# Kernel tuning notes

Measured on AMD Instinct MI355X. Metric: run time of the kernel, lower is better.

The kernel has to match this reference:

```python
import jax, jax.numpy as jnp
import numpy as np

EXCHANGE_RATIO = 0.5


def setup_inputs() -> dict:
    key = jax.random.key(0)
    k1, k2, k3, k4 = jax.random.split(key, 4)
    B, C, L = 8, 512, 4096
    x1 = jax.random.normal(k1, (B, C, L), dtype=jnp.float32)
    x2 = jax.random.normal(k2, (B, C, L), dtype=jnp.float32)
    bn1 = jax.random.normal(k3, (C,), dtype=jnp.float32)
    bn2 = jax.random.normal(k4, (C,), dtype=jnp.float32)
    return {"x1": x1, "x2": x2, "bn1": bn1, "bn2": bn2}


def _nontop_indices(bn, topk):
    # channels NOT in topk of |bn|, in ascending index order (matches torch
    # boolean-mask indexing semantics)
    a = jnp.abs(bn)
    C = bn.shape[0]
    _, idx = jax.lax.top_k(a, topk)
    mask = jnp.zeros((C,), dtype=bool).at[idx].set(True)
    # stable argsort of bool puts False (non-top) first, in ascending index order
    nontop = jnp.argsort(mask, stable=True)[: C - topk]
    return nontop


def reference(x1, x2, bn1, bn2):
    C = bn1.shape[0]
    topk = int(C * (1.0 - EXCHANGE_RATIO))  # static: 256
    nontop1 = _nontop_indices(bn1, topk)
    nontop2 = _nontop_indices(bn2, topk)
    # y1 keeps x1's top channels, takes x2's non-top channels (order-aligned)
    y1 = x1.at[:, nontop1, :].set(x2[:, nontop2, :])
    # y2 keeps x2's top channels, takes x1's non-top channels
    y2 = x2.at[:, nontop2, :].set(x1[:, nontop1, :])
    return (y1, y2)
```

## Files before the change

kernel.cpp:

```cpp
#include <hip/hip_runtime.h>
#include <math.h>

#define C_CH   512
#define TOPK   256
#define B_N    8
#define L_LEN  4096
#define L4     (L_LEN / 4)
#define NVEC   (B_N * C_CH * L4)

__global__ void build_maps(const float* __restrict__ bn1,
                           const float* __restrict__ bn2,
                           int* __restrict__ map1,
                           int* __restrict__ map2) {
    __shared__ float a1[C_CH], a2[C_CH];
    __shared__ int istop1[C_CH], istop2[C_CH];
    __shared__ int nontop1[C_CH], nontop2[C_CH];
    const int t = threadIdx.x;
    a1[t] = fabsf(bn1[t]);
    a2[t] = fabsf(bn2[t]);
    __syncthreads();

    const float v1 = a1[t], v2 = a2[t];
    int r1 = 0, r2 = 0;
    for (int j = 0; j < C_CH; ++j) {
        const float b1 = a1[j], b2 = a2[j];
        r1 += (b1 > v1) || (b1 == v1 && j < t);
        r2 += (b2 > v2) || (b2 == v2 && j < t);
    }
    const int top1 = (r1 < TOPK);
    const int top2 = (r2 < TOPK);
    istop1[t] = top1;
    istop2[t] = top2;
    __syncthreads();

    int p1 = -1, p2 = -1;
    if (!top1) {
        int p = 0;
        for (int j = 0; j < t; ++j) p += !istop1[j];
        p1 = p;
        nontop1[p] = t;
    }
    if (!top2) {
        int p = 0;
        for (int j = 0; j < t; ++j) p += !istop2[j];
        p2 = p;
        nontop2[p] = t;
    }
    __syncthreads();

    map1[t] = top1 ? t : (C_CH + nontop2[p1]);
    map2[t] = top2 ? t : (C_CH + nontop1[p2]);
}

__global__ __launch_bounds__(256) void exchange_copy(
        const float4* __restrict__ x1,
        const float4* __restrict__ x2,
        const int* __restrict__ map1,
        const int* __restrict__ map2,
        float4* __restrict__ y1,
        float4* __restrict__ y2) {
    const int idx = blockIdx.x * blockDim.x + threadIdx.x;
    const int off = idx & (L4 - 1);
    const int row = idx >> 10;
    const int c   = row & (C_CH - 1);
    const int b   = row >> 9;

    const int m1 = map1[c];
    const int m2 = map2[c];

    const float4* s1 = (m1 < C_CH) ? x1 : x2;
    const float4* s2 = (m2 < C_CH) ? x2 : x1;
    const int c1 = m1 & (C_CH - 1);
    const int c2 = m2 & (C_CH - 1);

    const int base_b = b << 9;
    y1[idx] = s1[(((base_b | c1) << 10) | off)];
    y2[idx] = s2[(((base_b | c2) << 10) | off)];
}

extern "C" void kernel_launch(void* const* d_in, const int* in_sizes, int n_in,
                              void* d_out, int out_size, void* d_ws, size_t ws_size,
                              hipStream_t stream) {
    const float* x1  = (const float*)d_in[0];
    const float* x2  = (const float*)d_in[1];
    const float* bn1 = (const float*)d_in[2];
    const float* bn2 = (const float*)d_in[3];

    float* y1 = (float*)d_out;
    float* y2 = (float*)d_out + (B_N * C_CH * L_LEN);

    int* map1 = (int*)d_ws;
    int* map2 = map1 + C_CH;

    build_maps<<<1, C_CH, 0, stream>>>(bn1, bn2, map1, map2);

    const int threads = 256;
    const int blocks = NVEC / threads;
    exchange_copy<<<blocks, threads, 0, stream>>>(
        (const float4*)x1, (const float4*)x2, map1, map2,
        (float4*)y1, (float4*)y2);
}
```

Before: 275.8 us.

## Use ballot prefix sums in map build and row-per-block batched copy

The map-building kernel now finds the position of each non-top channel with wavefront ballot, popcount and a small per-wave prefix sum, replacing the O(C) serial scan in each thread, and packs the two abs arrays into one float2 shared array. The copy kernel gives each block one full row, so the map lookup happens once per row, and each thread issues four float4 loads per source before storing them, raising memory-level parallelism. The grid shrinks to 4096 blocks, each doing more work per thread, which may reduce latency hiding if occupancy limits the number of loads in flight.

```diff
diff --git a/kernel.cpp b/kernel.cpp
--- a/kernel.cpp
+++ b/kernel.cpp
@@ -6,50 +6,54 @@
 #define B_N    8
 #define L_LEN  4096
 #define L4     (L_LEN / 4)
-#define NVEC   (B_N * C_CH * L4)
+#define ROWS   (B_N * C_CH)
 
-__global__ void build_maps(const float* __restrict__ bn1,
-                           const float* __restrict__ bn2,
-                           int* __restrict__ map1,
-                           int* __restrict__ map2) {
-    __shared__ float a1[C_CH], a2[C_CH];
-    __shared__ int istop1[C_CH], istop2[C_CH];
-    __shared__ int nontop1[C_CH], nontop2[C_CH];
+__global__ __launch_bounds__(C_CH) void build_maps(
+        const float* __restrict__ bn1,
+        const float* __restrict__ bn2,
+        int* __restrict__ map1,
+        int* __restrict__ map2) {
+    __shared__ float2 a12[C_CH];
+    __shared__ int nt1[C_CH - TOPK], nt2[C_CH - TOPK];
+    __shared__ int wsum1[8], wsum2[8];
     const int t = threadIdx.x;
-    a1[t] = fabsf(bn1[t]);
-    a2[t] = fabsf(bn2[t]);
+    const float v1 = fabsf(bn1[t]);
+    const float v2 = fabsf(bn2[t]);
+    a12[t] = make_float2(v1, v2);
     __syncthreads();
 
-    const float v1 = a1[t], v2 = a2[t];
     int r1 = 0, r2 = 0;
+#pragma unroll 8
     for (int j = 0; j < C_CH; ++j) {
-        const float b1 = a1[j], b2 = a2[j];
-        r1 += (b1 > v1) || (b1 == v1 && j < t);
-        r2 += (b2 > v2) || (b2 == v2 && j < t);
+        const float2 bj = a12[j];
+        r1 += (bj.x > v1) || (bj.x == v1 && j < t);
+        r2 += (bj.y > v2) || (bj.y == v2 && j < t);
     }
-    const int top1 = (r1 < TOPK);
-    const int top2 = (r2 < TOPK);
-    istop1[t] = top1;
-    istop2[t] = top2;
+    const bool non1 = (r1 >= TOPK);
+    const bool non2 = (r2 >= TOPK);
+
+    const unsigned long long m1 = __ballot(non1);
+    const unsigned long long m2 = __ballot(non2);
+    const int lane = t & 63, w = t >> 6;
+    const unsigned long long below = (1ULL << lane) - 1ULL;
+    const int lp1 = __popcll(m1 & below);
+    const int lp2 = __popcll(m2 & below);
+    if (lane == 0) { wsum1[w] = __popcll(m1); wsum2[w] = __popcll(m2); }
+    __syncthreads();
+    int base1 = 0, base2 = 0;
+#pragma unroll
+    for (int i = 0; i < 8; ++i) {
+        base1 += (i < w) ? wsum1[i] : 0;
+        base2 += (i < w) ? wsum2[i] : 0;
+    }
+    const int p1 = base1 + lp1;
+    const int p2 = base2 + lp2;
+    if (non1) nt1[p1] = t;
+    if (non2) nt2[p2] = t;
     __syncthreads();
 
-    int p1 = -1, p2 = -1;
-    if (!top1) {
-        int p = 0;
-        for (int j = 0; j < t; ++j) p += !istop1[j];
-        p1 = p;
-        nontop1[p] = t;
-    }
-    if (!top2) {
-        int p = 0;
-        for (int j = 0; j < t; ++j) p += !istop2[j];
-        p2 = p;
-        nontop2[p] = t;
-    }
-    __syncthreads();
-
-    map1[t] = top1 ? t : (C_CH + nontop2[p1]);
-    map2[t] = top2 ? t : (C_CH + nontop1[p2]);
+    map1[t] = non1 ? (C_CH + nt2[p1]) : t;
+    map2[t] = non2 ? (C_CH + nt1[p2]) : t;
 }
 
 __global__ __launch_bounds__(256) void exchange_copy(
@@ -59,23 +63,33 @@
         const int* __restrict__ map2,
         float4* __restrict__ y1,
         float4* __restrict__ y2) {
-    const int idx = blockIdx.x * blockDim.x + threadIdx.x;
-    const int off = idx & (L4 - 1);
-    const int row = idx >> 10;
-    const int c   = row & (C_CH - 1);
-    const int b   = row >> 9;
+    const int row = blockIdx.x;
+    const int c = row & (C_CH - 1);
+    const int b = row >> 9;
 
     const int m1 = map1[c];
     const int m2 = map2[c];
+    const float4* __restrict__ s1 = (m1 < C_CH) ? x1 : x2;
+    const float4* __restrict__ s2 = (m2 < C_CH) ? x2 : x1;
+    const size_t src1 = (size_t)((b << 9) | (m1 & (C_CH - 1))) << 10;
+    const size_t src2 = (size_t)((b << 9) | (m2 & (C_CH - 1))) << 10;
+    const size_t dst  = (size_t)row << 10;
 
-    const float4* s1 = (m1 < C_CH) ? x1 : x2;
-    const float4* s2 = (m2 < C_CH) ? x2 : x1;
-    const int c1 = m1 & (C_CH - 1);
-    const int c2 = m2 & (C_CH - 1);
+    const float4* __restrict__ p1 = s1 + src1;
+    const float4* __restrict__ p2 = s2 + src2;
+    float4* __restrict__ q1 = y1 + dst;
+    float4* __restrict__ q2 = y2 + dst;
 
-    const int base_b = b << 9;
-    y1[idx] = s1[(((base_b | c1) << 10) | off)];
-    y2[idx] = s2[(((base_b | c2) << 10) | off)];
+    const int t = threadIdx.x;
+    float4 r[4], s[4];
+#pragma unroll
+    for (int k = 0; k < 4; ++k) r[k] = p1[t + 256 * k];
+#pragma unroll
+    for (int k = 0; k < 4; ++k) s[k] = p2[t + 256 * k];
+#pragma unroll
+    for (int k = 0; k < 4; ++k) q1[t + 256 * k] = r[k];
+#pragma unroll
+    for (int k = 0; k < 4; ++k) q2[t + 256 * k] = s[k];
 }
 
 extern "C" void kernel_launch(void* const* d_in, const int* in_sizes, int n_in,
@@ -94,9 +108,7 @@
 
     build_maps<<<1, C_CH, 0, stream>>>(bn1, bn2, map1, map2);
 
-    const int threads = 256;
-    const int blocks = NVEC / threads;
-    exchange_copy<<<blocks, threads, 0, stream>>>(
+    exchange_copy<<<ROWS, 256, 0, stream>>>(
         (const float4*)x1, (const float4*)x2, map1, map2,
         (float4*)y1, (float4*)y2);
 }
```

Measured after the change: 265.5 us. 1.04x faster.
